# Optimization experiments

Hardware: AMD Instinct MI355X
Metric: run time of the kernel (lower is better)

Reference implementation:

```python
import jax, jax.numpy as jnp
import numpy as np

B, L, H, E = 16, 2048, 8, 64   # batch, seq_len, heads, head_dim (= in_ch//8 = out_ch//8)
IN_CH, OUT_CH = 512, 512
MODES = 64


def setup_inputs() -> dict:
    key = jax.random.key(0)
    ks = jax.random.split(key, 11)
    scale = 1.0 / (IN_CH * OUT_CH)
    inv_sqrt_e = E ** -0.5
    return {
        "q": jax.random.normal(ks[0], (B, L, H, E), jnp.float32),
        "k": jax.random.normal(ks[1], (B, L, H, E), jnp.float32),
        "v": jax.random.normal(ks[2], (B, L, H, E), jnp.float32),
        "wq_w": jax.random.normal(ks[3], (E, E), jnp.float32) * inv_sqrt_e,
        "wq_b": jax.random.normal(ks[4], (E,), jnp.float32) * 0.01,
        "wk_w": jax.random.normal(ks[5], (E, E), jnp.float32) * inv_sqrt_e,
        "wk_b": jax.random.normal(ks[6], (E,), jnp.float32) * 0.01,
        "wv_w": jax.random.normal(ks[7], (E, E), jnp.float32) * inv_sqrt_e,
        "wv_b": jax.random.normal(ks[8], (E,), jnp.float32) * 0.01,
        "weights1": scale * jax.random.uniform(ks[9], (8, IN_CH // 8, OUT_CH // 8, MODES), jnp.float32),
        "weights2": scale * jax.random.uniform(ks[10], (8, IN_CH // 8, OUT_CH // 8, MODES), jnp.float32),
        "index_q": jnp.arange(MODES, dtype=jnp.int32),   # 'else' mode-select: lowest modes
        "index_kv": jnp.arange(MODES, dtype=jnp.int32),
    }


def reference(q, k, v, wq_w, wq_b, wk_w, wk_b, wv_w, wv_b,
              weights1, weights2, index_q, index_kv):
    # per-head linear projections (torch Linear: x @ W.T + b), on last dim E
    q = q @ wq_w.T + wq_b
    k = k @ wk_w.T + wk_b
    v = v @ wv_w.T + wv_b  # v is projected but unused downstream (faithful to source)

    # [B, L, H, E] -> [B, H, E, L]
    xq = jnp.transpose(q, (0, 2, 3, 1))
    xk = jnp.transpose(k, (0, 2, 3, 1))

    # rFFT along sequence, then gather the selected sparse frequency modes
    xq_ft = jnp.fft.rfft(xq, axis=-1)          # [B, H, E, L//2+1] complex
    xk_ft = jnp.fft.rfft(xk, axis=-1)
    xq_sel = xq_ft[..., index_q]               # [B, H, E, Mq]
    xk_sel = xk_ft[..., index_kv]              # [B, H, E, Mkv]

    # frequency-domain attention scores (plain complex product, no conjugate)
    xqk_ft = jnp.einsum('bhex,bhey->bhxy', xq_sel, xk_sel)
    # 'tanh' activation applied separately to real and imag parts
    xqk_ft = jnp.tanh(xqk_ft.real) + 1j * jnp.tanh(xqk_ft.imag)

    xqkv_ft = jnp.einsum('bhxy,bhey->bhex', xqk_ft, xk_sel)     # [B, H, E, Mq]
    w = weights1 + 1j * weights2                                # [8, E, O, Mq]
    xqkvw = jnp.einsum('bhex,heox->bhox', xqkv_ft, w.astype(jnp.complex64))

    # scatter selected modes back into zero spectrum, then inverse rFFT
    n_freq = L // 2 + 1
    out_ft = jnp.zeros((B, H, OUT_CH // 8, n_freq), dtype=jnp.complex64)
    out_ft = out_ft.at[..., index_q].set(xqkvw)
    out = jnp.fft.irfft(out_ft / IN_CH / OUT_CH, n=L, axis=-1)  # [B, H, O, L]
    return out
```

## Files before the change

kernel.cpp:

```cpp
#include <hip/hip_runtime.h>
#include <math.h>

#define Lseq 2048

#define OFF_TWQ 0u
#define OFF_TWK (256u << 10)
#define OFF_GQ  (1u << 20)
#define OFF_GK  (5u << 20)
#define OFF_U   (9u << 20)
#define OFF_A   (13u << 20)
#define OFF_GP  (17u << 20)
#define OFF_WC  (17u << 20)

__global__ __launch_bounds__(256) void k_twiddle(
    const int* __restrict__ iq, const int* __restrict__ ikv,
    float2* __restrict__ twq, float2* __restrict__ twk)
{
    int idx = blockIdx.x * 256 + threadIdx.x;
    int t = idx >> 6;
    int m = idx & 63;
    const float w = 6.2831853071795864769f / (float)Lseq;
    float s, c;
    int ph = (t * iq[m]) & (Lseq - 1);
    sincosf(w * (float)ph, &s, &c);
    twq[idx] = make_float2(c, s);
    ph = (t * ikv[m]) & (Lseq - 1);
    sincosf(w * (float)ph, &s, &c);
    twk[idx] = make_float2(c, s);
}

__global__ __launch_bounds__(256) void k_wtrans(
    const float* __restrict__ w1, const float* __restrict__ w2,
    float2* __restrict__ wc)
{
    int h = blockIdx.x, e = blockIdx.y;
    const float* p1 = w1 + (((size_t)h * 64 + e) * 64) * 64;
    const float* p2 = w2 + (((size_t)h * 64 + e) * 64) * 64;
    __shared__ float s1[64][65];
    __shared__ float s2[64][65];
    int tid = threadIdx.x;
    for (int i = tid; i < 1024; i += 256) {
        int o = i >> 4, xc = (i & 15) * 4;
        float4 a = *(const float4*)(p1 + o * 64 + xc);
        s1[o][xc] = a.x; s1[o][xc + 1] = a.y; s1[o][xc + 2] = a.z; s1[o][xc + 3] = a.w;
        float4 b = *(const float4*)(p2 + o * 64 + xc);
        s2[o][xc] = b.x; s2[o][xc + 1] = b.y; s2[o][xc + 2] = b.z; s2[o][xc + 3] = b.w;
    }
    __syncthreads();
    float2* dst = wc + ((size_t)h * 64) * 4096 + (size_t)e * 64;
    for (int i = tid; i < 4096; i += 256) {
        int x = i >> 6, o = i & 63;
        dst[(size_t)x * 4096 + o] = make_float2(s1[o][x], s2[o][x]);
    }
}

__global__ __launch_bounds__(512) void k_dft(
    const float* __restrict__ q, const float* __restrict__ k,
    const float* __restrict__ twq, const float* __restrict__ twk,
    float2* __restrict__ Gp)
{
    int b = blockIdx.x, h = blockIdx.y, zc = blockIdx.z;
    int z = zc >> 1, chunk = zc & 1;
    const float* src = z ? k : q;
    const float* tws = z ? twk : twq;

    __shared__ float y_s[2][16][4][64];
    __shared__ float tw_s[2][16][144];

    int tid = threadIdx.x;
    int sub = tid >> 8;
    int st  = tid & 255;
    int eg = st >> 4, g = st & 15;
    int t_base = chunk * 256 + sub * 128;
    const float* xbase = src + ((size_t)b * Lseq) * 512 + h * 64;
    int goff = g * 8 + ((g >> 2) << 2);

    float a[4][12];
#pragma unroll
    for (int i = 0; i < 4; ++i)
#pragma unroll
        for (int j = 0; j < 12; ++j) a[i][j] = 0.f;

    for (int rnd = 0; rnd < 8; ++rnd) {
        int t0 = t_base + rnd * 16;
        {
            int tl = st >> 4, e4 = (st & 15) * 4;
            const float* p = xbase + (size_t)(t0 + tl) * 512 + e4;
            float4 v0 = *(const float4*)(p);
            float4 v1 = *(const float4*)(p + 512 * 512);
            float4 v2 = *(const float4*)(p + 1024 * 512);
            float4 v3 = *(const float4*)(p + 1536 * 512);
            float4 sa, sb, y0, y2, pp, qq;
            sa.x = v0.x + v2.x; sa.y = v0.y + v2.y; sa.z = v0.z + v2.z; sa.w = v0.w + v2.w;
            sb.x = v1.x + v3.x; sb.y = v1.y + v3.y; sb.z = v1.z + v3.z; sb.w = v1.w + v3.w;
            y0.x = sa.x + sb.x; y0.y = sa.y + sb.y; y0.z = sa.z + sb.z; y0.w = sa.w + sb.w;
            y2.x = sa.x - sb.x; y2.y = sa.y - sb.y; y2.z = sa.z - sb.z; y2.w = sa.w - sb.w;
            pp.x = v0.x - v2.x; pp.y = v0.y - v2.y; pp.z = v0.z - v2.z; pp.w = v0.w - v2.w;
            qq.x = v1.x - v3.x; qq.y = v1.y - v3.y; qq.z = v1.z - v3.z; qq.w = v1.w - v3.w;
            *(float4*)&y_s[sub][tl][0][e4] = y0;
            *(float4*)&y_s[sub][tl][1][e4] = y2;
            *(float4*)&y_s[sub][tl][2][e4] = pp;
            *(float4*)&y_s[sub][tl][3][e4] = qq;
        }
        {
#pragma unroll
            for (int u = 0; u < 2; ++u) {
                int i = st * 2 + u;
                int tl = i >> 5, rem = i & 31, gg = rem >> 1, half = rem & 1;
                float4 w = *(const float4*)(tws + (size_t)(t0 + tl) * 128 + gg * 8 + half * 4);
                *(float4*)&tw_s[sub][tl][gg * 8 + ((gg >> 2) << 2) + half * 4] = w;
            }
        }
        __syncthreads();
#pragma unroll
        for (int tt = 0; tt < 16; ++tt) {
            float4 Y0 = *(float4*)&y_s[sub][tt][0][eg * 4];
            float4 Y2 = *(float4*)&y_s[sub][tt][1][eg * 4];
            float4 Pv = *(float4*)&y_s[sub][tt][2][eg * 4];
            float4 Qv = *(float4*)&y_s[sub][tt][3][eg * 4];
            float4 w0 = *(float4*)&tw_s[sub][tt][goff];
            float4 w1 = *(float4*)&tw_s[sub][tt][goff + 4];
            const float* y0a = (const float*)&Y0;
            const float* y2a = (const float*)&Y2;
            const float* pa  = (const float*)&Pv;
            const float* qa  = (const float*)&Qv;
#pragma unroll
            for (int i = 0; i < 4; ++i) {
                a[i][0]  += y0a[i] * w0.x;  a[i][1]  += y0a[i] * w0.y;
                a[i][2]  += y2a[i] * w1.x;  a[i][3]  += y2a[i] * w1.y;
                a[i][4]  += pa[i]  * w0.z;  a[i][5]  += qa[i]  * w0.w;
                a[i][6]  += pa[i]  * w0.w;  a[i][7]  += qa[i]  * w0.z;
                a[i][8]  += pa[i]  * w1.z;  a[i][9]  += qa[i]  * w1.w;
                a[i][10] += pa[i]  * w1.w;  a[i][11] += qa[i]  * w1.z;
            }
        }
        __syncthreads();
    }

    float gv[32];
#pragma unroll
    for (int i = 0; i < 4; ++i) {
        gv[i * 8 + 0] = a[i][0];
        gv[i * 8 + 1] = -a[i][1];
        gv[i * 8 + 2] = a[i][4] - a[i][5];
        gv[i * 8 + 3] = -(a[i][6] + a[i][7]);
        gv[i * 8 + 4] = a[i][2];
        gv[i * 8 + 5] = -a[i][3];
        gv[i * 8 + 6] = a[i][8] + a[i][9];
        gv[i * 8 + 7] = a[i][11] - a[i][10];
    }

    float4* red = (float4*)y_s;
    float4* gvf = (float4*)gv;
    if (sub == 1) {
#pragma unroll
        for (int j = 0; j < 8; ++j) red[st * 8 + (j ^ (st & 7))] = gvf[j];
    }
    __syncthreads();
    if (sub == 0) {
        int slot = ((z * 16 + b) * 8 + h) * 2 + chunk;
        float4* gp = (float4*)(Gp + (size_t)slot * 4096);
#pragma unroll
        for (int j = 0; j < 8; ++j) {
            float4 r = red[st * 8 + (j ^ (st & 7))];
            float4 v = gvf[j];
            v.x += r.x; v.y += r.y; v.z += r.z; v.w += r.w;
            int i = j >> 1, half = j & 1;
            gp[(eg * 4 + i) * 32 + 2 * g + half] = v;
        }
    }
}

__global__ __launch_bounds__(256) void k_reduce(
    const float4* __restrict__ Gp, float4* __restrict__ Gq, float4* __restrict__ Gk)
{
    int gid = blockIdx.x * 256 + threadIdx.x;
#pragma unroll
    for (int kk = 0; kk < 4; ++kk) {
        int f4 = gid + kk * 131072;
        int zbh = f4 >> 11, pos = f4 & 2047;
        const float4* s = Gp + (size_t)(zbh * 2) * 2048;
        float4 x0 = s[pos], x1 = s[2048 + pos];
        x0.x += x1.x; x0.y += x1.y; x0.z += x1.z; x0.w += x1.w;
        float4* dst = (zbh < 128) ? Gq : Gk;
        dst[(size_t)(zbh & 127) * 2048 + pos] = x0;
    }
}

__global__ __launch_bounds__(256) void k_core(
    const float2* __restrict__ Gq, const float2* __restrict__ Gk,
    const float* __restrict__ wqw, const float* __restrict__ wqb,
    const float* __restrict__ wkw, const float* __restrict__ wkb,
    const int* __restrict__ iq, const int* __restrict__ ikv,
    float2* __restrict__ U)
{
    int b = blockIdx.x, h = blockIdx.y;
    int tid = threadIdx.x;
    __shared__ float2 bufA[4096];
    __shared__ float2 Qf[4096];
    __shared__ float2 Kf[4096];
    __shared__ float  Wm[4096];
    __shared__ float  bias_s[64];
    __shared__ int    idx_s[64];

    size_t gb = (size_t)(b * 8 + h) * 4096;

    for (int z = 0; z < 2; ++z) {
        const float* Wsrc = z ? wkw : wqw;
        const float* bsrc = z ? wkb : wqb;
        const int*   isrc = z ? ikv : iq;
        const float2* Gsrc = (z ? Gk : Gq) + gb;
        float2* dst = z ? Kf : Qf;
        if (tid < 64) { bias_s[tid] = bsrc[tid]; idx_s[tid] = isrc[tid]; }
#pragma unroll
        for (int j = 0; j < 4; ++j)
            ((float4*)Wm)[tid + 256 * j] = ((const float4*)Wsrc)[tid + 256 * j];
#pragma unroll
        for (int j = 0; j < 8; ++j)
            ((float4*)bufA)[tid + 256 * j] = ((const float4*)Gsrc)[tid + 256 * j];
        __syncthreads();
        {
            int eg = tid >> 4, xg = tid & 15;
            float2 acc[4][4];
#pragma unroll
            for (int i = 0; i < 4; ++i)
#pragma unroll
                for (int j = 0; j < 4; ++j) acc[i][j] = make_float2(0.f, 0.f);
            for (int ep = 0; ep < 64; ++ep) {
                float wv[4]; float2 gvv[4];
#pragma unroll
                for (int i = 0; i < 4; ++i) wv[i] = Wm[(eg * 4 + i) * 64 + ep];
#pragma unroll
                for (int j = 0; j < 4; ++j) gvv[j] = bufA[ep * 64 + xg + 16 * j];
#pragma unroll
                for (int i = 0; i < 4; ++i)
#pragma unroll
                    for (int j = 0; j < 4; ++j) {
                        acc[i][j].x += wv[i] * gvv[j].x;
                        acc[i][j].y += wv[i] * gvv[j].y;
                    }
            }
#pragma unroll
            for (int j = 0; j < 4; ++j) {
                int x = xg + 16 * j;
                float bz = (idx_s[x] == 0) ? 2048.0f : 0.0f;
#pragma unroll
                for (int i = 0; i < 4; ++i) {
                    float2 v = acc[i][j];
                    v.x += bz * bias_s[eg * 4 + i];
                    dst[(eg * 4 + i) * 64 + x] = v;
                }
            }
        }
        __syncthreads();
    }

    {
        int xg = tid & 15, yg = tid >> 4;
        float2 acc[4][4];
#pragma unroll
        for (int i = 0; i < 4; ++i)
#pragma unroll
            for (int j = 0; j < 4; ++j) acc[i][j] = make_float2(0.f, 0.f);
        for (int e = 0; e < 64; ++e) {
            float2 qv[4], kv[4];
#pragma unroll
            for (int i = 0; i < 4; ++i) qv[i] = Qf[e * 64 + xg + 16 * i];
#pragma unroll
            for (int j = 0; j < 4; ++j) kv[j] = Kf[e * 64 + yg * 4 + j];
#pragma unroll
            for (int i = 0; i < 4; ++i)
#pragma unroll
                for (int j = 0; j < 4; ++j) {
                    acc[i][j].x += qv[i].x * kv[j].x - qv[i].y * kv[j].y;
                    acc[i][j].y += qv[i].x * kv[j].y + qv[i].y * kv[j].x;
                }
        }
#pragma unroll
        for (int i = 0; i < 4; ++i)
#pragma unroll
            for (int j = 0; j < 4; ++j)
                bufA[(yg * 4 + j) * 64 + xg + 16 * i] =
                    make_float2(tanhf(acc[i][j].x), tanhf(acc[i][j].y));
    }
    __syncthreads();

    {
        int xg = tid & 15, eg = tid >> 4;
        float2 acc[4][4];
#pragma unroll
        for (int i = 0; i < 4; ++i)
#pragma unroll
            for (int j = 0; j < 4; ++j) acc[i][j] = make_float2(0.f, 0.f);
        for (int y = 0; y < 64; ++y) {
            float2 kv[4], tv[4];
#pragma unroll
            for (int i = 0; i < 4; ++i) kv[i] = Kf[(eg * 4 + i) * 64 + y];
#pragma unroll
            for (int j = 0; j < 4; ++j) tv[j] = bufA[y * 64 + xg + 16 * j];
#pragma unroll
            for (int i = 0; i < 4; ++i)
#pragma unroll
                for (int j = 0; j < 4; ++j) {
                    acc[i][j].x += tv[j].x * kv[i].x - tv[j].y * kv[i].y;
                    acc[i][j].y += tv[j].x * kv[i].y + tv[j].y * kv[i].x;
                }
        }
        float2* Ud = U + gb;
#pragma unroll
        for (int i = 0; i < 4; ++i)
#pragma unroll
            for (int j = 0; j < 4; ++j)
                Ud[(eg * 4 + i) * 64 + xg + 16 * j] = acc[i][j];
    }
}

__global__ __launch_bounds__(128) void k_apply_w(
    const float2* __restrict__ U, const float2* __restrict__ wc,
    const int* __restrict__ iq, float2* __restrict__ A)
{
    int x = blockIdx.x, h = blockIdx.y;
    int tid = threadIdx.x;
    __shared__ float2 wl[4096];
    __shared__ float2 ul[16][65];
    const float4* wsrc = (const float4*)(wc + (size_t)(h * 64 + x) * 4096);
#pragma unroll
    for (int j = 0; j < 16; ++j)
        ((float4*)wl)[tid + 128 * j] = wsrc[tid + 128 * j];
#pragma unroll
    for (int j = 0; j < 8; ++j) {
        int idx = tid + 128 * j;
        int bb = idx >> 6, e = idx & 63;
        ul[bb][e] = U[((size_t)(bb * 8 + h) * 64 + e) * 64 + x];
    }
    __syncthreads();
    int bb = tid >> 3, og = tid & 7;
    float2 acc[8];
#pragma unroll
    for (int j = 0; j < 8; ++j) acc[j] = make_float2(0.f, 0.f);
    for (int e = 0; e < 64; ++e) {
        float2 u = ul[bb][e];
#pragma unroll
        for (int j = 0; j < 8; ++j) {
            float2 wv = wl[e * 64 + og + 8 * j];
            acc[j].x += u.x * wv.x - u.y * wv.y;
            acc[j].y += u.x * wv.y + u.y * wv.x;
        }
    }
    int f = iq[x];
    bool dc = (f == 0) || (2 * f == Lseq);
    float cm = (dc ? 1.0f : 2.0f) * (1.0f / (2048.0f * 262144.0f));
    float2* Ad = A + (size_t)(bb * 8 + h) * 4096;
#pragma unroll
    for (int j = 0; j < 8; ++j) {
        int o = og + 8 * j;
        Ad[o * 64 + x] = make_float2(cm * acc[j].x, dc ? 0.0f : -cm * acc[j].y);
    }
}

__global__ __launch_bounds__(512) void k_irfft(
    const float2* __restrict__ A, const float* __restrict__ tw,
    float* __restrict__ out)
{
    int tt = blockIdx.x, h = blockIdx.y, b = blockIdx.z;
    int t0 = tt * 64;
    int tid = threadIdx.x;
    __shared__ float2 A_s[4096];
    __shared__ float  tw_s[64][128];
    const float4* asrc = (const float4*)(A + (size_t)(b * 8 + h) * 4096);
#pragma unroll
    for (int j = 0; j < 4; ++j)
        ((float4*)A_s)[tid + 512 * j] = asrc[tid + 512 * j];
    {
        int row = tid >> 3, c4b = (tid & 7) * 4;
        const float4* s = (const float4*)(tw + (size_t)(t0 + row) * 128);
        float4* drow = (float4*)&tw_s[row][0];
#pragma unroll
        for (int kk = 0; kk < 4; ++kk) {
            int c4 = c4b + kk;
            drow[c4 ^ (row & 31)] = s[c4];
        }
    }
    __syncthreads();
    int tl = tid & 63, ow = tid >> 6;
    float U0[8], U1[8], V1[8], U2[8], U3[8], V3[8];
#pragma unroll
    for (int i = 0; i < 8; ++i) { U0[i]=U1[i]=V1[i]=U2[i]=U3[i]=V3[i]=0.f; }
    const float4* trow = (const float4*)&tw_s[tl][0];
    int sw = tl & 31;
#pragma unroll
    for (int g = 0; g < 16; ++g) {
        float4 w0 = trow[(2 * g) ^ sw];
        float4 w1 = trow[(2 * g + 1) ^ sw];
#pragma unroll
        for (int i = 0; i < 8; ++i) {
            const float4* ap = (const float4*)&A_s[(ow * 8 + i) * 64 + 4 * g];
            float4 a0 = ap[0];
            float4 a1 = ap[1];
            U0[i] += a0.x * w0.x + a0.y * w0.y;
            U1[i] += a0.z * w0.z + a0.w * w0.w;
            V1[i] += a0.w * w0.z - a0.z * w0.w;
            U2[i] += a1.x * w1.x + a1.y * w1.y;
            U3[i] += a1.z * w1.z + a1.w * w1.w;
            V3[i] += a1.w * w1.z - a1.z * w1.w;
        }
    }
    float* op = out + ((size_t)(b * 8 + h) * 64 + ow * 8) * Lseq + t0 + tl;
#pragma unroll
    for (int i = 0; i < 8; ++i) {
        float u0 = U0[i], u1 = U1[i], v1 = V1[i], u2 = U2[i], u3 = U3[i], v3 = V3[i];
        op[(size_t)i * Lseq +    0] = u0 + u1 + u2 + u3;
        op[(size_t)i * Lseq +  512] = u0 + v1 - u2 - v3;
        op[(size_t)i * Lseq + 1024] = u0 - u1 + u2 - u3;
        op[(size_t)i * Lseq + 1536] = u0 - v1 - u2 + v3;
    }
}

extern "C" void kernel_launch(void* const* d_in, const int* in_sizes, int n_in,
                              void* d_out, int out_size, void* d_ws, size_t ws_size,
                              hipStream_t stream)
{
    const float* q    = (const float*)d_in[0];
    const float* k    = (const float*)d_in[1];
    const float* wq_w = (const float*)d_in[3];
    const float* wq_b = (const float*)d_in[4];
    const float* wk_w = (const float*)d_in[5];
    const float* wk_b = (const float*)d_in[6];
    const float* w1   = (const float*)d_in[9];
    const float* w2   = (const float*)d_in[10];
    const int*   iq   = (const int*)d_in[11];
    const int*   ikv  = (const int*)d_in[12];
    float* out = (float*)d_out;

    char* ws = (char*)d_ws;
    float2* twq = (float2*)(ws + OFF_TWQ);
    float2* twk = (float2*)(ws + OFF_TWK);
    float2* Gq  = (float2*)(ws + OFF_GQ);
    float2* Gk  = (float2*)(ws + OFF_GK);
    float2* Uw  = (float2*)(ws + OFF_U);
    float2* Aw  = (float2*)(ws + OFF_A);
    float2* Gp  = (float2*)(ws + OFF_GP);
    float2* wc  = (float2*)(ws + OFF_WC);

    k_twiddle<<<128, 256, 0, stream>>>(iq, ikv, twq, twk);
    k_dft<<<dim3(16, 8, 4), 512, 0, stream>>>(q, k, (const float*)twq,
                                              (const float*)twk, Gp);
    k_reduce<<<512, 256, 0, stream>>>((const float4*)Gp, (float4*)Gq, (float4*)Gk);
    k_core<<<dim3(16, 8), 256, 0, stream>>>(Gq, Gk, wq_w, wq_b, wk_w, wk_b,
                                            iq, ikv, Uw);
    k_wtrans<<<dim3(8, 64), 256, 0, stream>>>(w1, w2, wc);
    k_apply_w<<<dim3(64, 8), 128, 0, stream>>>(Uw, wc, iq, Aw);
    k_irfft<<<dim3(8, 8, 16), 512, 0, stream>>>(Aw, (const float*)twq, out);
}
```

Baseline: 377.2 us.

## Restructure DFT kernel: drop partial reduce, register-prefetch inputs, recurrent twiddles

The DFT kernel now processes a whole (b,h,z) slice per block instead of splitting it into two chunks. This removes the Gp partial buffer and the separate k_reduce launch, with a 4-way shared-memory reduction across sub-groups replacing them. Inputs and twiddles are register-prefetched for the next round into double-buffered shared memory, so there is one barrier per round. Twiddles are no longer staged in LDS: each thread holds 16 modes and advances them with a complex rotation recurrence per time step. The cost is half as many blocks (256), more registers (two 48-float accumulator sets) and a small precision drift from the recurrence.

```diff
diff --git a/kernel.cpp b/kernel.cpp
--- a/kernel.cpp
+++ b/kernel.cpp
@@ -9,7 +9,6 @@
 #define OFF_GK  (5u << 20)
 #define OFF_U   (9u << 20)
 #define OFF_A   (13u << 20)
-#define OFF_GP  (17u << 20)
 #define OFF_WC  (17u << 20)
 
 __global__ __launch_bounds__(256) void k_twiddle(
@@ -54,136 +53,174 @@
     }
 }
 
-__global__ __launch_bounds__(512) void k_dft(
+__global__ __launch_bounds__(512, 2) void k_dft(
     const float* __restrict__ q, const float* __restrict__ k,
     const float* __restrict__ twq, const float* __restrict__ twk,
-    float2* __restrict__ Gp)
-{
-    int b = blockIdx.x, h = blockIdx.y, zc = blockIdx.z;
-    int z = zc >> 1, chunk = zc & 1;
+    float2* __restrict__ Gq, float2* __restrict__ Gk)
+{
+    int b = blockIdx.x, h = blockIdx.y, z = blockIdx.z;
     const float* src = z ? k : q;
     const float* tws = z ? twk : twq;
 
-    __shared__ float y_s[2][16][4][64];
-    __shared__ float tw_s[2][16][144];
+    __shared__ float y_s[2][4][8][4][64];
 
     int tid = threadIdx.x;
-    int sub = tid >> 8;
-    int st  = tid & 255;
-    int eg = st >> 4, g = st & 15;
-    int t_base = chunk * 256 + sub * 128;
+    int sub = tid >> 7;
+    int st  = tid & 127;
+    int tl  = st >> 4;
+    int e4q = st & 15;
+    int eg  = st >> 3;
+    int g8  = st & 7;
+    int tbase = sub * 128;
+
     const float* xbase = src + ((size_t)b * Lseq) * 512 + h * 64;
-    int goff = g * 8 + ((g >> 2) << 2);
-
-    float a[4][12];
+    const float* xrow0 = xbase + (size_t)(tbase + tl) * 512 + e4q * 4;
+
+    const float* trow1 = tws + 128 + g8 * 16;
+    float4 d0 = *(const float4*)(trow1);
+    float4 d1 = *(const float4*)(trow1 + 4);
+    float4 d2 = *(const float4*)(trow1 + 8);
+    float4 d3 = *(const float4*)(trow1 + 12);
+    float dc[8], dsn[8];
+    dc[0] = d0.x; dsn[0] = d0.y; dc[1] = d0.z; dsn[1] = d0.w;
+    dc[2] = d1.x; dsn[2] = d1.y; dc[3] = d1.z; dsn[3] = d1.w;
+    dc[4] = d2.x; dsn[4] = d2.y; dc[5] = d2.z; dsn[5] = d2.w;
+    dc[6] = d3.x; dsn[6] = d3.y; dc[7] = d3.z; dsn[7] = d3.w;
+
+    float a[4][12], bb[4][12];
 #pragma unroll
     for (int i = 0; i < 4; ++i)
 #pragma unroll
-        for (int j = 0; j < 12; ++j) a[i][j] = 0.f;
-
-    for (int rnd = 0; rnd < 8; ++rnd) {
-        int t0 = t_base + rnd * 16;
+        for (int j = 0; j < 12; ++j) { a[i][j] = 0.f; bb[i][j] = 0.f; }
+
+    float4 c0 = *(const float4*)(xrow0);
+    float4 c1 = *(const float4*)(xrow0 + 262144);
+    float4 c2 = *(const float4*)(xrow0 + 524288);
+    float4 c3 = *(const float4*)(xrow0 + 786432);
+    const float* trow = tws + (size_t)tbase * 128 + g8 * 16;
+    float4 tA = *(const float4*)(trow);
+    float4 tB = *(const float4*)(trow + 4);
+    float4 tC = *(const float4*)(trow + 8);
+    float4 tD = *(const float4*)(trow + 12);
+    float4 n0, n1, n2, n3, uA, uB, uC, uD;
+
+    for (int rnd = 0; rnd < 16; ++rnd) {
+        int buf = rnd & 1;
         {
-            int tl = st >> 4, e4 = (st & 15) * 4;
-            const float* p = xbase + (size_t)(t0 + tl) * 512 + e4;
-            float4 v0 = *(const float4*)(p);
-            float4 v1 = *(const float4*)(p + 512 * 512);
-            float4 v2 = *(const float4*)(p + 1024 * 512);
-            float4 v3 = *(const float4*)(p + 1536 * 512);
             float4 sa, sb, y0, y2, pp, qq;
-            sa.x = v0.x + v2.x; sa.y = v0.y + v2.y; sa.z = v0.z + v2.z; sa.w = v0.w + v2.w;
-            sb.x = v1.x + v3.x; sb.y = v1.y + v3.y; sb.z = v1.z + v3.z; sb.w = v1.w + v3.w;
+            sa.x = c0.x + c2.x; sa.y = c0.y + c2.y; sa.z = c0.z + c2.z; sa.w = c0.w + c2.w;
+            sb.x = c1.x + c3.x; sb.y = c1.y + c3.y; sb.z = c1.z + c3.z; sb.w = c1.w + c3.w;
             y0.x = sa.x + sb.x; y0.y = sa.y + sb.y; y0.z = sa.z + sb.z; y0.w = sa.w + sb.w;
             y2.x = sa.x - sb.x; y2.y = sa.y - sb.y; y2.z = sa.z - sb.z; y2.w = sa.w - sb.w;
-            pp.x = v0.x - v2.x; pp.y = v0.y - v2.y; pp.z = v0.z - v2.z; pp.w = v0.w - v2.w;
-            qq.x = v1.x - v3.x; qq.y = v1.y - v3.y; qq.z = v1.z - v3.z; qq.w = v1.w - v3.w;
-            *(float4*)&y_s[sub][tl][0][e4] = y0;
-            *(float4*)&y_s[sub][tl][1][e4] = y2;
-            *(float4*)&y_s[sub][tl][2][e4] = pp;
-            *(float4*)&y_s[sub][tl][3][e4] = qq;
-        }
-        {
-#pragma unroll
-            for (int u = 0; u < 2; ++u) {
-                int i = st * 2 + u;
-                int tl = i >> 5, rem = i & 31, gg = rem >> 1, half = rem & 1;
-                float4 w = *(const float4*)(tws + (size_t)(t0 + tl) * 128 + gg * 8 + half * 4);
-                *(float4*)&tw_s[sub][tl][gg * 8 + ((gg >> 2) << 2) + half * 4] = w;
-            }
+            pp.x = c0.x - c2.x; pp.y = c0.y - c2.y; pp.z = c0.z - c2.z; pp.w = c0.w - c2.w;
+            qq.x = c1.x - c3.x; qq.y = c1.y - c3.y; qq.z = c1.z - c3.z; qq.w = c1.w - c3.w;
+            *(float4*)&y_s[buf][sub][tl][0][e4q * 4] = y0;
+            *(float4*)&y_s[buf][sub][tl][1][e4q * 4] = y2;
+            *(float4*)&y_s[buf][sub][tl][2][e4q * 4] = pp;
+            *(float4*)&y_s[buf][sub][tl][3][e4q * 4] = qq;
         }
         __syncthreads();
-#pragma unroll
-        for (int tt = 0; tt < 16; ++tt) {
-            float4 Y0 = *(float4*)&y_s[sub][tt][0][eg * 4];
-            float4 Y2 = *(float4*)&y_s[sub][tt][1][eg * 4];
-            float4 Pv = *(float4*)&y_s[sub][tt][2][eg * 4];
-            float4 Qv = *(float4*)&y_s[sub][tt][3][eg * 4];
-            float4 w0 = *(float4*)&tw_s[sub][tt][goff];
-            float4 w1 = *(float4*)&tw_s[sub][tt][goff + 4];
+        if (rnd < 15) {
+            const float* p = xrow0 + (size_t)(rnd + 1) * (8 * 512);
+            n0 = *(const float4*)(p);
+            n1 = *(const float4*)(p + 262144);
+            n2 = *(const float4*)(p + 524288);
+            n3 = *(const float4*)(p + 786432);
+            const float* tr = tws + (size_t)(tbase + (rnd + 1) * 8) * 128 + g8 * 16;
+            uA = *(const float4*)(tr);
+            uB = *(const float4*)(tr + 4);
+            uC = *(const float4*)(tr + 8);
+            uD = *(const float4*)(tr + 12);
+        }
+        float wc_[8], ws_[8];
+        wc_[0] = tA.x; ws_[0] = tA.y; wc_[1] = tA.z; ws_[1] = tA.w;
+        wc_[2] = tB.x; ws_[2] = tB.y; wc_[3] = tB.z; ws_[3] = tB.w;
+        wc_[4] = tC.x; ws_[4] = tC.y; wc_[5] = tC.z; ws_[5] = tC.w;
+        wc_[6] = tD.x; ws_[6] = tD.y; wc_[7] = tD.z; ws_[7] = tD.w;
+#pragma unroll
+        for (int tt = 0; tt < 8; ++tt) {
+            float4 Y0 = *(float4*)&y_s[buf][sub][tt][0][eg * 4];
+            float4 Y2 = *(float4*)&y_s[buf][sub][tt][1][eg * 4];
+            float4 Pv = *(float4*)&y_s[buf][sub][tt][2][eg * 4];
+            float4 Qv = *(float4*)&y_s[buf][sub][tt][3][eg * 4];
             const float* y0a = (const float*)&Y0;
             const float* y2a = (const float*)&Y2;
             const float* pa  = (const float*)&Pv;
             const float* qa  = (const float*)&Qv;
 #pragma unroll
             for (int i = 0; i < 4; ++i) {
-                a[i][0]  += y0a[i] * w0.x;  a[i][1]  += y0a[i] * w0.y;
-                a[i][2]  += y2a[i] * w1.x;  a[i][3]  += y2a[i] * w1.y;
-                a[i][4]  += pa[i]  * w0.z;  a[i][5]  += qa[i]  * w0.w;
-                a[i][6]  += pa[i]  * w0.w;  a[i][7]  += qa[i]  * w0.z;
-                a[i][8]  += pa[i]  * w1.z;  a[i][9]  += qa[i]  * w1.w;
-                a[i][10] += pa[i]  * w1.w;  a[i][11] += qa[i]  * w1.z;
+                a[i][0]  += y0a[i] * wc_[0];  a[i][1]  += y0a[i] * ws_[0];
+                a[i][2]  += y2a[i] * wc_[2];  a[i][3]  += y2a[i] * ws_[2];
+                a[i][4]  += pa[i]  * wc_[1];  a[i][5]  += qa[i]  * ws_[1];
+                a[i][6]  += pa[i]  * ws_[1];  a[i][7]  += qa[i]  * wc_[1];
+                a[i][8]  += pa[i]  * wc_[3];  a[i][9]  += qa[i]  * ws_[3];
+                a[i][10] += pa[i]  * ws_[3];  a[i][11] += qa[i]  * wc_[3];
+                bb[i][0]  += y0a[i] * wc_[4];  bb[i][1]  += y0a[i] * ws_[4];
+                bb[i][2]  += y2a[i] * wc_[6];  bb[i][3]  += y2a[i] * ws_[6];
+                bb[i][4]  += pa[i]  * wc_[5];  bb[i][5]  += qa[i]  * ws_[5];
+                bb[i][6]  += pa[i]  * ws_[5];  bb[i][7]  += qa[i]  * wc_[5];
+                bb[i][8]  += pa[i]  * wc_[7];  bb[i][9]  += qa[i]  * ws_[7];
+                bb[i][10] += pa[i]  * ws_[7];  bb[i][11] += qa[i]  * wc_[7];
             }
-        }
-        __syncthreads();
-    }
-
-    float gv[32];
+            if (tt < 7) {
+#pragma unroll
+                for (int m = 0; m < 8; ++m) {
+                    float c = wc_[m], s = ws_[m];
+                    wc_[m] = c * dc[m] - s * dsn[m];
+                    ws_[m] = s * dc[m] + c * dsn[m];
+                }
+            }
+        }
+        if (rnd < 15) {
+            c0 = n0; c1 = n1; c2 = n2; c3 = n3;
+            tA = uA; tB = uB; tC = uC; tD = uD;
+        }
+    }
+
+    __syncthreads();
+
+    float4 gvf[16];
 #pragma unroll
     for (int i = 0; i < 4; ++i) {
-        gv[i * 8 + 0] = a[i][0];
-        gv[i * 8 + 1] = -a[i][1];
-        gv[i * 8 + 2] = a[i][4] - a[i][5];
-        gv[i * 8 + 3] = -(a[i][6] + a[i][7]);
-        gv[i * 8 + 4] = a[i][2];
-        gv[i * 8 + 5] = -a[i][3];
-        gv[i * 8 + 6] = a[i][8] + a[i][9];
-        gv[i * 8 + 7] = a[i][11] - a[i][10];
+        gvf[i * 4 + 0] = make_float4(a[i][0], -a[i][1], a[i][4] - a[i][5], -(a[i][6] + a[i][7]));
+        gvf[i * 4 + 1] = make_float4(a[i][2], -a[i][3], a[i][8] + a[i][9], a[i][11] - a[i][10]);
+        gvf[i * 4 + 2] = make_float4(bb[i][0], -bb[i][1], bb[i][4] - bb[i][5], -(bb[i][6] + bb[i][7]));
+        gvf[i * 4 + 3] = make_float4(bb[i][2], -bb[i][3], bb[i][8] + bb[i][9], bb[i][11] - bb[i][10]);
     }
 
     float4* red = (float4*)y_s;
-    float4* gvf = (float4*)gv;
-    if (sub == 1) {
-#pragma unroll
-        for (int j = 0; j < 8; ++j) red[st * 8 + (j ^ (st & 7))] = gvf[j];
+    int rbase = ((sub >> 1) * 128 + st) * 16;
+    int sx = st & 15;
+    if (sub & 1) {
+#pragma unroll
+        for (int j = 0; j < 16; ++j) red[rbase + (j ^ sx)] = gvf[j];
+    }
+    __syncthreads();
+    if (!(sub & 1)) {
+#pragma unroll
+        for (int j = 0; j < 16; ++j) {
+            float4 r = red[rbase + (j ^ sx)];
+            gvf[j].x += r.x; gvf[j].y += r.y; gvf[j].z += r.z; gvf[j].w += r.w;
+        }
+    }
+    __syncthreads();
+    if (sub == 2) {
+#pragma unroll
+        for (int j = 0; j < 16; ++j) red[st * 16 + (j ^ sx)] = gvf[j];
     }
     __syncthreads();
     if (sub == 0) {
-        int slot = ((z * 16 + b) * 8 + h) * 2 + chunk;
-        float4* gp = (float4*)(Gp + (size_t)slot * 4096);
-#pragma unroll
-        for (int j = 0; j < 8; ++j) {
-            float4 r = red[st * 8 + (j ^ (st & 7))];
-            float4 v = gvf[j];
-            v.x += r.x; v.y += r.y; v.z += r.z; v.w += r.w;
-            int i = j >> 1, half = j & 1;
-            gp[(eg * 4 + i) * 32 + 2 * g + half] = v;
-        }
-    }
-}
-
-__global__ __launch_bounds__(256) void k_reduce(
-    const float4* __restrict__ Gp, float4* __restrict__ Gq, float4* __restrict__ Gk)
-{
-    int gid = blockIdx.x * 256 + threadIdx.x;
-#pragma unroll
-    for (int kk = 0; kk < 4; ++kk) {
-        int f4 = gid + kk * 131072;
-        int zbh = f4 >> 11, pos = f4 & 2047;
-        const float4* s = Gp + (size_t)(zbh * 2) * 2048;
-        float4 x0 = s[pos], x1 = s[2048 + pos];
-        x0.x += x1.x; x0.y += x1.y; x0.z += x1.z; x0.w += x1.w;
-        float4* dst = (zbh < 128) ? Gq : Gk;
-        dst[(size_t)(zbh & 127) * 2048 + pos] = x0;
+#pragma unroll
+        for (int j = 0; j < 16; ++j) {
+            float4 r = red[st * 16 + (j ^ sx)];
+            gvf[j].x += r.x; gvf[j].y += r.y; gvf[j].z += r.z; gvf[j].w += r.w;
+        }
+        float4* Gd4 = (float4*)((z ? Gk : Gq) + (size_t)(b * 8 + h) * 4096);
+#pragma unroll
+        for (int i = 0; i < 4; ++i)
+#pragma unroll
+            for (int j4 = 0; j4 < 4; ++j4)
+                Gd4[(eg * 4 + i) * 32 + g8 * 4 + j4] = gvf[i * 4 + j4];
     }
 }
 
@@ -439,13 +476,11 @@
     float2* Gk  = (float2*)(ws + OFF_GK);
     float2* Uw  = (float2*)(ws + OFF_U);
     float2* Aw  = (float2*)(ws + OFF_A);
-    float2* Gp  = (float2*)(ws + OFF_GP);
     float2* wc  = (float2*)(ws + OFF_WC);
 
     k_twiddle<<<128, 256, 0, stream>>>(iq, ikv, twq, twk);
-    k_dft<<<dim3(16, 8, 4), 512, 0, stream>>>(q, k, (const float*)twq,
-                                              (const float*)twk, Gp);
-    k_reduce<<<512, 256, 0, stream>>>((const float4*)Gp, (float4*)Gq, (float4*)Gk);
+    k_dft<<<dim3(16, 8, 2), 512, 0, stream>>>(q, k, (const float*)twq,
+                                              (const float*)twk, Gq, Gk);
     k_core<<<dim3(16, 8), 256, 0, stream>>>(Gq, Gk, wq_w, wq_b, wk_w, wk_b,
                                             iq, ikv, Uw);
     k_wtrans<<<dim3(8, 64), 256, 0, stream>>>(w1, w2, wc);
```

Result: slower. 789.7 us (+109.3%).
